# Optimization experiments

Hardware: AMD Instinct MI355X
Metric: run time of the kernel (lower is better)

Reference implementation:

```python
import jax, jax.numpy as jnp
import numpy as np

N_NODES = 50000
N_EDGES = 800000
IN_DIM = 256
OUT_DIM = 128


def setup_inputs() -> dict:
    key = jax.random.key(0)
    k1, k2, k3, k4, k5 = jax.random.split(key, 5)
    adj_rows = jax.random.randint(k1, (N_EDGES,), 0, N_NODES, dtype=jnp.int32)
    adj_cols = jax.random.randint(k2, (N_EDGES,), 0, N_NODES, dtype=jnp.int32)
    adj_vals = jax.random.uniform(k3, (N_EDGES,), dtype=jnp.float32)
    x = jax.random.normal(k4, (N_NODES, IN_DIM), dtype=jnp.float32)
    # kaiming_normal-ish init for weight
    W = jax.random.normal(k5, (IN_DIM, OUT_DIM), dtype=jnp.float32) * np.sqrt(2.0 / IN_DIM)
    b = jnp.zeros((OUT_DIM,), dtype=jnp.float32)
    return {"adj_rows": adj_rows, "adj_cols": adj_cols, "adj_vals": adj_vals,
            "x": x, "W": W, "b": b}


def reference(adj_rows, adj_cols, adj_vals, x, W, b):
    # support = X @ W  (dense GEMM)
    support = x @ W  # [N, OUT_DIM]
    # sparse A @ support via edge-parallel gather + segment-sum (COO SpMM)
    msgs = adj_vals[:, None] * support[adj_cols]  # [E, OUT_DIM]
    out = jax.ops.segment_sum(msgs, adj_rows, num_segments=x.shape[0])
    return out + b
```

## Files before the change

kernel.cpp:

```cpp
#include <hip/hip_runtime.h>
#include <hip/hip_bf16.h>

#define N_NODES 50000
#define N_EDGES 800000
#define IN_DIM  256
#define OUT_DIM 128

#define NBINS        256
#define ROWS_PER_BIN 196
#define BIN_CAP      3600
#define EPB          2048
#define NB_BIN       391
#define NB_GEMM      782
#define CUR_STRIDE   32

typedef __bf16 bf16x8 __attribute__((ext_vector_type(8)));
typedef float  f32x4  __attribute__((ext_vector_type(4)));

__device__ __forceinline__ unsigned bin_of(unsigned r) { return (r * 85599u) >> 24; }
__device__ __forceinline__ float blo(unsigned u) { return __uint_as_float(u << 16); }
__device__ __forceinline__ float bhi(unsigned u) { return __uint_as_float(u & 0xffff0000u); }

#define WT_OFF   0
#define SUP_OFF  65536
#define BIN_OFF  12865536
#define CUR_OFF  20238336

__global__ void k_prep(const float* __restrict__ W, __bf16* __restrict__ Wt,
                       int* __restrict__ bin_cursor) {
    int t = blockIdx.x * 256 + threadIdx.x;
    if (t < 32768) { int n = t >> 8, k = t & 255; Wt[t] = (__bf16)W[k * OUT_DIM + n]; }
    if (t < NBINS) bin_cursor[t * CUR_STRIDE] = t * BIN_CAP;
}

__global__ __launch_bounds__(256) void k_fused(const float* __restrict__ x,
                                               const __bf16* __restrict__ Wt,
                                               unsigned* __restrict__ sup32,
                                               const int* __restrict__ rows,
                                               const int* __restrict__ cols,
                                               const float* __restrict__ vals,
                                               int* __restrict__ bin_cursor,
                                               int2* __restrict__ binbuf) {
    __shared__ int s_cur[NBINS];
    __shared__ int s_base[NBINS];
    int t = threadIdx.x;

    if (blockIdx.x < NB_BIN) {
        long e0 = (long)blockIdx.x * EPB;
        s_cur[t] = 0;
        __syncthreads();

        int2 rec[8];
        int  lrank[8];
        bool full = (e0 + EPB <= N_EDGES);

        if (full) {
#pragma unroll
            for (int k = 0; k < 8; ++k) {
                long e = e0 + k * 256 + t;
                unsigned r = (unsigned)rows[e];
                unsigned c = (unsigned)cols[e];
                float    w = vals[e];
                rec[k]   = make_int2((int)((r << 16) | c), __float_as_int(w));
                lrank[k] = atomicAdd(&s_cur[bin_of(r)], 1);
            }
        } else {
#pragma unroll
            for (int k = 0; k < 8; ++k) {
                long e = e0 + k * 256 + t;
                lrank[k] = -1;
                if (e < N_EDGES) {
                    unsigned r = (unsigned)rows[e];
                    unsigned c = (unsigned)cols[e];
                    float    w = vals[e];
                    rec[k]   = make_int2((int)((r << 16) | c), __float_as_int(w));
                    lrank[k] = atomicAdd(&s_cur[bin_of(r)], 1);
                }
            }
        }
        __syncthreads();

        s_base[t] = atomicAdd(&bin_cursor[t * CUR_STRIDE], s_cur[t]);
        __syncthreads();

        if (full) {
#pragma unroll
            for (int k = 0; k < 8; ++k) {
                unsigned bn = bin_of(((unsigned)rec[k].x) >> 16);
                int dst = s_base[bn] + lrank[k];
                if (dst < (int)(bn + 1) * BIN_CAP)
                    binbuf[dst] = rec[k];
            }
        } else {
#pragma unroll
            for (int k = 0; k < 8; ++k) {
                if (lrank[k] >= 0) {
                    unsigned bn = bin_of(((unsigned)rec[k].x) >> 16);
                    int dst = s_base[bn] + lrank[k];
                    if (dst < (int)(bn + 1) * BIN_CAP)
                        binbuf[dst] = rec[k];
                }
            }
        }
    } else {
        int  gb   = blockIdx.x - NB_BIN;
        int  wave = t >> 6;
        int  lane = t & 63;
        int  tile = gb * 4 + wave;
        if (tile >= 3125) return;
        int  m    = lane & 15;
        int  quad = lane >> 4;

        const float*  aprow = x  + ((long)tile * 16 + m) * IN_DIM + quad * 8;
        const __bf16* wpB   = Wt + m * IN_DIM + quad * 8;

        float4 fa[16];
#pragma unroll
        for (int ks = 0; ks < 8; ++ks) {
            fa[2 * ks]     = *(const float4*)(aprow + ks * 32);
            fa[2 * ks + 1] = *(const float4*)(aprow + ks * 32 + 4);
        }

        f32x4 acc[8];
#pragma unroll
        for (int n = 0; n < 8; ++n) acc[n] = (f32x4){0, 0, 0, 0};

#pragma unroll
        for (int ks = 0; ks < 8; ++ks) {
            float4 f0 = fa[2 * ks];
            float4 f1 = fa[2 * ks + 1];
            __bf16 c0 = (__bf16)f0.x, c1 = (__bf16)f0.y;
            __bf16 c2 = (__bf16)f0.z, c3 = (__bf16)f0.w;
            __bf16 c4 = (__bf16)f1.x, c5 = (__bf16)f1.y;
            __bf16 c6 = (__bf16)f1.z, c7 = (__bf16)f1.w;
            bf16x8 af = (bf16x8){c0, c1, c2, c3, c4, c5, c6, c7};
#pragma unroll
            for (int n = 0; n < 8; ++n) {
                bf16x8 bfr = *(const bf16x8*)(wpB + n * 16 * IN_DIM + ks * 32);
                acc[n] = __builtin_amdgcn_mfma_f32_16x16x32_bf16(af, bfr, acc[n], 0, 0, 0);
            }
        }

        unsigned* op = sup32 + (long)tile * 16 * 64;
#pragma unroll
        for (int r = 0; r < 4; ++r) {
#pragma unroll
            for (int n = 0; n < 4; ++n) {
                __bf16 lo = (__bf16)acc[n][r], hi = (__bf16)acc[n + 4][r];
                unsigned w = (unsigned)*(unsigned short*)&lo |
                             ((unsigned)*(unsigned short*)&hi << 16);
                op[(quad * 4 + r) * 64 + n * 16 + m] = w;
            }
        }
    }
}

__global__ __launch_bounds__(1024) void k_sg(const int* __restrict__ bin_cursor,
                                             const int2* __restrict__ binbuf,
                                             const unsigned* __restrict__ sup,
                                             const float* __restrict__ bias,
                                             float* __restrict__ out) {
    __shared__ int2 stage[BIN_CAP];
    __shared__ int2 sorted_[BIN_CAP];
    __shared__ int  cnt[256], off[256], cur[256], s[256];
    int b = blockIdx.x, t = threadIdx.x;
    int row0 = b * ROWS_PER_BIN;

    int n = bin_cursor[b * CUR_STRIDE] - b * BIN_CAP;
    n = n < 0 ? 0 : (n > BIN_CAP ? BIN_CAP : n);
    const int2* seg = binbuf + (long)b * BIN_CAP;

    if (t < 256) cnt[t] = 0;
    __syncthreads();

    for (int i = t; i < n; i += 1024) {
        int2 rec = seg[i];
        stage[i] = rec;
        atomicAdd(&cnt[(int)(((unsigned)rec.x) >> 16) - row0], 1);
    }
    __syncthreads();

    int v = 0;
    if (t < 256) { v = cnt[t]; s[t] = v; }
    __syncthreads();
#pragma unroll
    for (int o = 1; o < 256; o <<= 1) {
        int xv = 0;
        if (t < 256 && t >= o) xv = s[t - o];
        __syncthreads();
        if (t < 256) s[t] += xv;
        __syncthreads();
    }
    if (t < 256) { off[t] = s[t] - v; cur[t] = 0; }
    __syncthreads();

    for (int i = t; i < n; i += 1024) {
        int2 rec = stage[i];
        int rl = (int)(((unsigned)rec.x) >> 16) - row0;
        sorted_[off[rl] + atomicAdd(&cur[rl], 1)] = rec;
    }
    __syncthreads();

    int wave = t >> 6, lane = t & 63;
    float bb0 = bias[lane], bb1 = bias[64 + lane];

    for (int rl = wave; rl < ROWS_PER_BIN; rl += 16) {
        int row = row0 + rl;
        if (row >= N_NODES) continue;
        int st = off[rl], nd = cnt[rl];
        float a0 = 0.f, a1 = 0.f;
        for (int i = 0; i < nd; i += 8) {
            int2 e[8]; unsigned u[8]; float vv[8];
#pragma unroll
            for (int j = 0; j < 8; ++j) {
                int ok = (i + j) < nd;
                e[j]  = sorted_[ok ? st + i + j : st];
                vv[j] = ok ? __int_as_float(e[j].y) : 0.f;
            }
#pragma unroll
            for (int j = 0; j < 8; ++j)
                u[j] = sup[(long)(((unsigned)e[j].x) & 0xffffu) * 64 + lane];
#pragma unroll
            for (int j = 0; j < 8; ++j) {
                a0 += vv[j] * blo(u[j]);
                a1 += vv[j] * bhi(u[j]);
            }
        }
        out[(long)row * 128 + lane]      = a0 + bb0;
        out[(long)row * 128 + 64 + lane] = a1 + bb1;
    }
}

extern "C" void kernel_launch(void* const* d_in, const int* in_sizes, int n_in,
                              void* d_out, int out_size, void* d_ws, size_t ws_size,
                              hipStream_t stream) {
    const int*   adj_rows = (const int*)  d_in[0];
    const int*   adj_cols = (const int*)  d_in[1];
    const float* adj_vals = (const float*)d_in[2];
    const float* x        = (const float*)d_in[3];
    const float* W        = (const float*)d_in[4];
    const float* b        = (const float*)d_in[5];
    float* out = (float*)d_out;

    char* ws = (char*)d_ws;
    __bf16*   Wt         = (__bf16*)  (ws + WT_OFF);
    unsigned* sup32      = (unsigned*)(ws + SUP_OFF);
    int2*     binbuf     = (int2*)    (ws + BIN_OFF);
    int*      bin_cursor = (int*)     (ws + CUR_OFF);

    k_prep <<<128, 256, 0, stream>>>(W, Wt, bin_cursor);
    k_fused<<<NB_BIN + NB_GEMM, 256, 0, stream>>>(x, Wt, sup32,
                                                  adj_rows, adj_cols, adj_vals,
                                                  bin_cursor, binbuf);
    k_sg   <<<NBINS, 1024, 0, stream>>>(bin_cursor, binbuf, sup32, b, out);
}
```

Measured before the change: 177.0 us.

## Split fused bin/GEMM kernel and stage fragment-ordered W in LDS

Splits the combined edge-binning and GEMM kernel into two separate launches, and pre-permutes W into MFMA fragment order so each GEMM block copies the full 64KB B matrix into shared memory once. Per-lane B reads then come from LDS instead of strided global loads. This trades away the concurrency of running binning alongside the GEMM, adds an extra launch, and the 64KB of LDS per block limits occupancy.

```diff
diff --git a/kernel.cpp b/kernel.cpp
--- a/kernel.cpp
+++ b/kernel.cpp
@@ -21,136 +21,148 @@
 __device__ __forceinline__ float blo(unsigned u) { return __uint_as_float(u << 16); }
 __device__ __forceinline__ float bhi(unsigned u) { return __uint_as_float(u & 0xffff0000u); }
 
-#define WT_OFF   0
+#define WF_OFF   0
 #define SUP_OFF  65536
 #define BIN_OFF  12865536
 #define CUR_OFF  20238336
 
-__global__ void k_prep(const float* __restrict__ W, __bf16* __restrict__ Wt,
+__global__ void k_prep(const float* __restrict__ W, __bf16* __restrict__ Wf,
                        int* __restrict__ bin_cursor) {
     int t = blockIdx.x * 256 + threadIdx.x;
-    if (t < 32768) { int n = t >> 8, k = t & 255; Wt[t] = (__bf16)W[k * OUT_DIM + n]; }
+    if (t < 32768) {
+        int s = t >> 3, j = t & 7;
+        int nrow = ((s >> 9) << 4) | (s & 15);
+        int k    = (((s >> 4) & 3) << 3) | (((s >> 6) & 7) << 5) | j;
+        Wf[t] = (__bf16)W[k * OUT_DIM + nrow];
+    }
     if (t < NBINS) bin_cursor[t * CUR_STRIDE] = t * BIN_CAP;
 }
 
-__global__ __launch_bounds__(256) void k_fused(const float* __restrict__ x,
-                                               const __bf16* __restrict__ Wt,
-                                               unsigned* __restrict__ sup32,
-                                               const int* __restrict__ rows,
-                                               const int* __restrict__ cols,
-                                               const float* __restrict__ vals,
-                                               int* __restrict__ bin_cursor,
-                                               int2* __restrict__ binbuf) {
+__global__ __launch_bounds__(256) void k_bin(const int* __restrict__ rows,
+                                             const int* __restrict__ cols,
+                                             const float* __restrict__ vals,
+                                             int* __restrict__ bin_cursor,
+                                             int2* __restrict__ binbuf) {
     __shared__ int s_cur[NBINS];
     __shared__ int s_base[NBINS];
     int t = threadIdx.x;
 
-    if (blockIdx.x < NB_BIN) {
-        long e0 = (long)blockIdx.x * EPB;
-        s_cur[t] = 0;
-        __syncthreads();
-
-        int2 rec[8];
-        int  lrank[8];
-        bool full = (e0 + EPB <= N_EDGES);
-
-        if (full) {
-#pragma unroll
-            for (int k = 0; k < 8; ++k) {
-                long e = e0 + k * 256 + t;
+    long e0 = (long)blockIdx.x * EPB;
+    s_cur[t] = 0;
+    __syncthreads();
+
+    int2 rec[8];
+    int  lrank[8];
+    bool full = (e0 + EPB <= N_EDGES);
+
+    if (full) {
+#pragma unroll
+        for (int k = 0; k < 8; ++k) {
+            long e = e0 + k * 256 + t;
+            unsigned r = (unsigned)rows[e];
+            unsigned c = (unsigned)cols[e];
+            float    w = vals[e];
+            rec[k]   = make_int2((int)((r << 16) | c), __float_as_int(w));
+            lrank[k] = atomicAdd(&s_cur[bin_of(r)], 1);
+        }
+    } else {
+#pragma unroll
+        for (int k = 0; k < 8; ++k) {
+            long e = e0 + k * 256 + t;
+            lrank[k] = -1;
+            if (e < N_EDGES) {
                 unsigned r = (unsigned)rows[e];
                 unsigned c = (unsigned)cols[e];
                 float    w = vals[e];
                 rec[k]   = make_int2((int)((r << 16) | c), __float_as_int(w));
                 lrank[k] = atomicAdd(&s_cur[bin_of(r)], 1);
             }
-        } else {
-#pragma unroll
-            for (int k = 0; k < 8; ++k) {
-                long e = e0 + k * 256 + t;
-                lrank[k] = -1;
-                if (e < N_EDGES) {
-                    unsigned r = (unsigned)rows[e];
-                    unsigned c = (unsigned)cols[e];
-                    float    w = vals[e];
-                    rec[k]   = make_int2((int)((r << 16) | c), __float_as_int(w));
-                    lrank[k] = atomicAdd(&s_cur[bin_of(r)], 1);
-                }
-            }
-        }
-        __syncthreads();
-
-        s_base[t] = atomicAdd(&bin_cursor[t * CUR_STRIDE], s_cur[t]);
-        __syncthreads();
-
-        if (full) {
-#pragma unroll
-            for (int k = 0; k < 8; ++k) {
+        }
+    }
+    __syncthreads();
+
+    s_base[t] = atomicAdd(&bin_cursor[t * CUR_STRIDE], s_cur[t]);
+    __syncthreads();
+
+    if (full) {
+#pragma unroll
+        for (int k = 0; k < 8; ++k) {
+            unsigned bn = bin_of(((unsigned)rec[k].x) >> 16);
+            int dst = s_base[bn] + lrank[k];
+            if (dst < (int)(bn + 1) * BIN_CAP)
+                binbuf[dst] = rec[k];
+        }
+    } else {
+#pragma unroll
+        for (int k = 0; k < 8; ++k) {
+            if (lrank[k] >= 0) {
                 unsigned bn = bin_of(((unsigned)rec[k].x) >> 16);
                 int dst = s_base[bn] + lrank[k];
                 if (dst < (int)(bn + 1) * BIN_CAP)
                     binbuf[dst] = rec[k];
             }
-        } else {
-#pragma unroll
-            for (int k = 0; k < 8; ++k) {
-                if (lrank[k] >= 0) {
-                    unsigned bn = bin_of(((unsigned)rec[k].x) >> 16);
-                    int dst = s_base[bn] + lrank[k];
-                    if (dst < (int)(bn + 1) * BIN_CAP)
-                        binbuf[dst] = rec[k];
-                }
-            }
-        }
-    } else {
-        int  gb   = blockIdx.x - NB_BIN;
-        int  wave = t >> 6;
-        int  lane = t & 63;
-        int  tile = gb * 4 + wave;
-        if (tile >= 3125) return;
-        int  m    = lane & 15;
-        int  quad = lane >> 4;
-
-        const float*  aprow = x  + ((long)tile * 16 + m) * IN_DIM + quad * 8;
-        const __bf16* wpB   = Wt + m * IN_DIM + quad * 8;
-
-        float4 fa[16];
-#pragma unroll
-        for (int ks = 0; ks < 8; ++ks) {
-            fa[2 * ks]     = *(const float4*)(aprow + ks * 32);
-            fa[2 * ks + 1] = *(const float4*)(aprow + ks * 32 + 4);
-        }
-
-        f32x4 acc[8];
-#pragma unroll
-        for (int n = 0; n < 8; ++n) acc[n] = (f32x4){0, 0, 0, 0};
-
-#pragma unroll
-        for (int ks = 0; ks < 8; ++ks) {
-            float4 f0 = fa[2 * ks];
-            float4 f1 = fa[2 * ks + 1];
-            __bf16 c0 = (__bf16)f0.x, c1 = (__bf16)f0.y;
-            __bf16 c2 = (__bf16)f0.z, c3 = (__bf16)f0.w;
-            __bf16 c4 = (__bf16)f1.x, c5 = (__bf16)f1.y;
-            __bf16 c6 = (__bf16)f1.z, c7 = (__bf16)f1.w;
-            bf16x8 af = (bf16x8){c0, c1, c2, c3, c4, c5, c6, c7};
-#pragma unroll
-            for (int n = 0; n < 8; ++n) {
-                bf16x8 bfr = *(const bf16x8*)(wpB + n * 16 * IN_DIM + ks * 32);
-                acc[n] = __builtin_amdgcn_mfma_f32_16x16x32_bf16(af, bfr, acc[n], 0, 0, 0);
-            }
-        }
-
-        unsigned* op = sup32 + (long)tile * 16 * 64;
-#pragma unroll
-        for (int r = 0; r < 4; ++r) {
-#pragma unroll
-            for (int n = 0; n < 4; ++n) {
-                __bf16 lo = (__bf16)acc[n][r], hi = (__bf16)acc[n + 4][r];
-                unsigned w = (unsigned)*(unsigned short*)&lo |
-                             ((unsigned)*(unsigned short*)&hi << 16);
-                op[(quad * 4 + r) * 64 + n * 16 + m] = w;
-            }
+        }
+    }
+}
+
+__global__ __launch_bounds__(256, 2) void k_gemm(const float* __restrict__ x,
+                                                 const __bf16* __restrict__ Wf,
+                                                 unsigned* __restrict__ sup32) {
+    __shared__ uint4 sB[4096];
+    int t = threadIdx.x;
+
+    const uint4* wf4 = (const uint4*)Wf;
+#pragma unroll
+    for (int r = 0; r < 16; ++r) sB[r * 256 + t] = wf4[r * 256 + t];
+    __syncthreads();
+
+    int  wave = t >> 6;
+    int  lane = t & 63;
+    long tile = (long)blockIdx.x * 4 + wave;
+    if (tile >= 3125) return;
+    int  m    = lane & 15;
+    int  quad = lane >> 4;
+
+    const float* aprow = x + (tile * 16 + m) * IN_DIM + quad * 8;
+
+    float4 fa[16];
+#pragma unroll
+    for (int ks = 0; ks < 8; ++ks) {
+        fa[2 * ks]     = *(const float4*)(aprow + ks * 32);
+        fa[2 * ks + 1] = *(const float4*)(aprow + ks * 32 + 4);
+    }
+    bf16x8 ab[8];
+#pragma unroll
+    for (int ks = 0; ks < 8; ++ks) {
+        float4 f0 = fa[2 * ks];
+        float4 f1 = fa[2 * ks + 1];
+        ab[ks] = (bf16x8){(__bf16)f0.x, (__bf16)f0.y, (__bf16)f0.z, (__bf16)f0.w,
+                          (__bf16)f1.x, (__bf16)f1.y, (__bf16)f1.z, (__bf16)f1.w};
+    }
+
+    f32x4 acc[8];
+#pragma unroll
+    for (int n = 0; n < 8; ++n) acc[n] = (f32x4){0, 0, 0, 0};
+
+    const __bf16* sbh = (const __bf16*)sB;
+#pragma unroll
+    for (int ks = 0; ks < 8; ++ks) {
+#pragma unroll
+        for (int n = 0; n < 8; ++n) {
+            bf16x8 bfr = *(const bf16x8*)(sbh + (((n * 8 + ks) * 64 + lane) << 3));
+            acc[n] = __builtin_amdgcn_mfma_f32_16x16x32_bf16(ab[ks], bfr, acc[n], 0, 0, 0);
+        }
+    }
+
+    unsigned* op = sup32 + (long)tile * 16 * 64;
+#pragma unroll
+    for (int r = 0; r < 4; ++r) {
+#pragma unroll
+        for (int n = 0; n < 4; ++n) {
+            __bf16 lo = (__bf16)acc[n][r], hi = (__bf16)acc[n + 4][r];
+            unsigned w = (unsigned)*(unsigned short*)&lo |
+                         ((unsigned)*(unsigned short*)&hi << 16);
+            op[(quad * 4 + r) * 64 + n * 16 + m] = w;
         }
     }
 }
@@ -243,14 +255,14 @@
     float* out = (float*)d_out;
 
     char* ws = (char*)d_ws;
-    __bf16*   Wt         = (__bf16*)  (ws + WT_OFF);
+    __bf16*   Wf         = (__bf16*)  (ws + WF_OFF);
     unsigned* sup32      = (unsigned*)(ws + SUP_OFF);
     int2*     binbuf     = (int2*)    (ws + BIN_OFF);
     int*      bin_cursor = (int*)     (ws + CUR_OFF);
 
-    k_prep <<<128, 256, 0, stream>>>(W, Wt, bin_cursor);
-    k_fused<<<NB_BIN + NB_GEMM, 256, 0, stream>>>(x, Wt, sup32,
-                                                  adj_rows, adj_cols, adj_vals,
-                                                  bin_cursor, binbuf);
-    k_sg   <<<NBINS, 1024, 0, stream>>>(bin_cursor, binbuf, sup32, b, out);
-}
+    k_prep<<<128, 256, 0, stream>>>(W, Wf, bin_cursor);
+    k_bin <<<NB_BIN, 256, 0, stream>>>(adj_rows, adj_cols, adj_vals,
+                                       bin_cursor, binbuf);
+    k_gemm<<<NB_GEMM, 256, 0, stream>>>(x, Wf, sup32);
+    k_sg  <<<NBINS, 1024, 0, stream>>>(bin_cursor, binbuf, sup32, b, out);
+}
```

Measured after the change: 160.5 us. 9.3% less time.
